# Kernel tuning notes

Hardware: AMD Instinct MI355X
Metric: run time of the kernel (lower is better)

The kernel has to match this reference:

```python
import jax, jax.numpy as jnp
import numpy as np

B, T, C = 1, 4096, 1024
NH, NKV, HD = 16, 4, 64
N_REP = NH // NKV
WIN = 1024
EPS = 1e-5
ROPE_THETA = 10000.0


def setup_inputs() -> dict:
    key = jax.random.key(0)
    ks = jax.random.split(key, 6)
    s = 1.0 / np.sqrt(C)
    x = jax.random.normal(ks[0], (B, T, C), jnp.float32)
    wq = jax.random.normal(ks[1], (NH * HD, C), jnp.float32) * s
    wk = jax.random.normal(ks[2], (NKV * HD, C), jnp.float32) * s
    wv = jax.random.normal(ks[3], (NKV * HD, C), jnp.float32) * s
    wo = jax.random.normal(ks[4], (C, NH * HD), jnp.float32) * (1.0 / np.sqrt(NH * HD))
    q_norm_w = jnp.ones((HD,), jnp.float32)
    k_norm_w = jnp.ones((HD,), jnp.float32)
    # RoPE tables: (T, HD//2)
    inv_freq = 1.0 / (ROPE_THETA ** (np.arange(0, HD, 2, dtype=np.float32) / HD))
    ang = np.outer(np.arange(T, dtype=np.float32), inv_freq)
    freqs_cos = jnp.asarray(np.cos(ang), jnp.float32)
    freqs_sin = jnp.asarray(np.sin(ang), jnp.float32)
    return {"x": x, "wq": wq, "wk": wk, "wv": wv, "wo": wo,
            "q_norm_w": q_norm_w, "k_norm_w": k_norm_w,
            "freqs_cos": freqs_cos, "freqs_sin": freqs_sin}


def _rmsnorm(v, w):
    # RMSNorm over last dim (per-head)
    return v * jax.lax.rsqrt(jnp.mean(v * v, axis=-1, keepdims=True) + EPS) * w


def _rope(v, cos, sin):
    # v: (B, T, H, HD); interleaved complex rotation, matching torch polar freqs_cis
    vr, vi = v[..., 0::2], v[..., 1::2]
    c = cos[None, :, None, :]
    s = sin[None, :, None, :]
    out_r = vr * c - vi * s
    out_i = vr * s + vi * c
    return jnp.stack([out_r, out_i], axis=-1).reshape(v.shape)


def reference(x, wq, wk, wv, wo, q_norm_w, k_norm_w, freqs_cos, freqs_sin):
    xq = jnp.einsum('btc,dc->btd', x, wq).reshape(B, T, NH, HD)
    xk = jnp.einsum('btc,dc->btd', x, wk).reshape(B, T, NKV, HD)
    xv = jnp.einsum('btc,dc->btd', x, wv).reshape(B, T, NKV, HD)
    # per-head QK RMSNorm
    xq = _rmsnorm(xq, q_norm_w)
    xk = _rmsnorm(xk, k_norm_w)
    # RoPE
    xq = _rope(xq, freqs_cos, freqs_sin)
    xk = _rope(xk, freqs_cos, freqs_sin)
    # GQA: expand kv heads
    xk = jnp.repeat(xk, N_REP, axis=2)  # (B, T, NH, HD)
    xv = jnp.repeat(xv, N_REP, axis=2)
    scale = 1.0 / np.sqrt(HD)
    scores = jnp.einsum('bthd,bshd->bhts', xq, xk) * scale
    i = jnp.arange(T)[:, None]
    j = jnp.arange(T)[None, :]
    mask = (i >= j) & (i - j < WIN)  # causal + sliding window
    scores = jnp.where(mask[None, None], scores, -jnp.inf)
    attn = jax.nn.softmax(scores, axis=-1)
    y = jnp.einsum('bhts,bshd->bthd', attn, xv).reshape(B, T, NH * HD)
    return jnp.einsum('btd,cd->btc', y, wo)
```

## Files before the change

### kernel.cpp

```cpp
#include <hip/hip_runtime.h>
#include <hip/hip_bf16.h>


#define WIN_SZ 1024

typedef __attribute__((ext_vector_type(8))) short short8;
typedef __attribute__((ext_vector_type(8))) unsigned short ushort8;
typedef __attribute__((ext_vector_type(4))) float f32x4;
typedef __attribute__((ext_vector_type(16))) float f32x16;

#define GLOAD_LDS16(g, s)                                              \
  __builtin_amdgcn_global_load_lds(                                    \
      (const __attribute__((address_space(1))) unsigned int*)(g),      \
      (__attribute__((address_space(3))) unsigned int*)(s), 16, 0, 0)

__device__ __forceinline__ unsigned short f2bf(float f) {
  union { float f; unsigned u; } v; v.f = f;
  unsigned r = v.u + 0x7fffu + ((v.u >> 16) & 1u);
  return (unsigned short)(r >> 16);
}

__device__ __forceinline__ unsigned pk2bf(float lo, float hi) {
  __hip_bfloat162 h = __float22bfloat162_rn(make_float2(lo, hi));
  union { __hip_bfloat162 h; unsigned u; } c; c.h = h; return c.u;
}

__device__ __forceinline__ short8 frag4(unsigned w0, unsigned w1, unsigned w2, unsigned w3) {
  union { unsigned u[4]; short8 s; } x;
  x.u[0] = w0; x.u[1] = w1; x.u[2] = w2; x.u[3] = w3; return x.s;
}

__global__ __launch_bounds__(256) void k_f2b_all(const float* __restrict__ x,
                                                 const float* __restrict__ wq,
                                                 const float* __restrict__ wk,
                                                 const float* __restrict__ wv,
                                                 const float* __restrict__ wo,
                                                 unsigned short* __restrict__ xb,
                                                 unsigned short* __restrict__ wqkvb,
                                                 unsigned short* __restrict__ wob) {
  int q = blockIdx.x * 256 + threadIdx.x;
  const float* src;
  unsigned short* dst;
  int off;
  if (q < 1048576) { src = x; dst = xb; off = q; }
  else if (q < 1310720) { src = wq; dst = wqkvb; off = q - 1048576; }
  else if (q < 1376256) { src = wk; dst = wqkvb + 1024 * 1024; off = q - 1310720; }
  else if (q < 1441792) { src = wv; dst = wqkvb + 1280 * 1024; off = q - 1376256; }
  else { src = wo; dst = wob; off = q - 1441792; }
  float4 v = ((const float4*)src)[off];
  ushort4 o;
  o.x = f2bf(v.x); o.y = f2bf(v.y); o.z = f2bf(v.z); o.w = f2bf(v.w);
  ((ushort4*)dst)[off] = o;
}

__global__ __launch_bounds__(256) void k_gemm_qkv(const unsigned short* __restrict__ A,
                                                  const unsigned short* __restrict__ B,
                                                  const float* __restrict__ qw,
                                                  const float* __restrict__ kw,
                                                  const float* __restrict__ fc,
                                                  const float* __restrict__ fs,
                                                  unsigned short* __restrict__ Qb,
                                                  unsigned short* __restrict__ Kb,
                                                  unsigned short* __restrict__ Vtg) {
  const int K = 1024;
  __shared__ unsigned short As[2][128 * 64];
  __shared__ unsigned short Bs[2][64 * 64];
  const int id = blockIdx.x;
  const int chunk = gridDim.x >> 3;
  const int swz = (id & 7) * chunk + (id >> 3);
  const int n_idx = swz % 24, m_idx = swz / 24;
  const int m0 = m_idx * 128, n0 = n_idx * 64;

  const int tid = threadIdx.x;
  const int w = tid >> 6, l = tid & 63;
  const int wr = w >> 1, wc = w & 1;
  const int r = l & 15, g = l >> 4;
  const int lr = l >> 3, lc = l & 7;
  const int srowb = w * 32, browb = w * 16;

  f32x4 acc[4][2];
#pragma unroll
  for (int i = 0; i < 4; i++)
#pragma unroll
    for (int j = 0; j < 2; j++) acc[i][j] = {0.f, 0.f, 0.f, 0.f};

  const unsigned short* Ag = A + (size_t)(m0 + srowb + lr) * K + lc * 8;
  const unsigned short* Bg = B + (size_t)(n0 + browb + lr) * K + lc * 8;

  auto stage = [&](int buf, int k0) {
#pragma unroll
    for (int it = 0; it < 4; it++)
      GLOAD_LDS16(Ag + (size_t)(it * 8) * K + k0, &As[buf][(srowb + it * 8) * 64]);
#pragma unroll
    for (int it = 0; it < 2; it++)
      GLOAD_LDS16(Bg + (size_t)(it * 8) * K + k0, &Bs[buf][(browb + it * 8) * 64]);
  };

  stage(0, 0);
  __syncthreads();
  int cur = 0;
  const int NT = K >> 6;
  for (int t = 0; t < NT; ++t) {
    if (t + 1 < NT) stage(cur ^ 1, (t + 1) << 6);
    const char* Ab = (const char*)As[cur];
    const char* Bb = (const char*)Bs[cur];
#pragma unroll
    for (int kk = 0; kk < 2; kk++) {
      short8 af[4], bfr[2];
#pragma unroll
      for (int mi = 0; mi < 4; mi++)
        af[mi] = *(const short8*)(Ab + (wr * 64 + mi * 16 + r) * 128 + kk * 64 + g * 16);
#pragma unroll
      for (int nj = 0; nj < 2; nj++)
        bfr[nj] = *(const short8*)(Bb + (wc * 32 + nj * 16 + r) * 128 + kk * 64 + g * 16);
#pragma unroll
      for (int mi = 0; mi < 4; mi++)
#pragma unroll
        for (int nj = 0; nj < 2; nj++)
          acc[mi][nj] = __builtin_amdgcn_mfma_f32_16x16x32_bf16(af[mi], bfr[nj], acc[mi][nj], 0, 0, 0);
    }
    __syncthreads();
    cur ^= 1;
  }

  const int u = n0 >> 6;
  if (u < 20) {
    float* ssb = (float*)As;
    f32x4 sv[4];
#pragma unroll
    for (int mi = 0; mi < 4; mi++) {
      f32x4 s;
#pragma unroll
      for (int e = 0; e < 4; e++)
        s[e] = acc[mi][0][e] * acc[mi][0][e] + acc[mi][1][e] * acc[mi][1][e];
#pragma unroll
      for (int off = 1; off < 16; off <<= 1)
#pragma unroll
        for (int e = 0; e < 4; e++) s[e] += __shfl_xor(s[e], off);
      sv[mi] = s;
    }
    if (r == 0) {
#pragma unroll
      for (int mi = 0; mi < 4; mi++)
#pragma unroll
        for (int e = 0; e < 4; e++)
          ssb[(wr * 64 + mi * 16 + g * 4 + e) * 2 + wc] = sv[mi][e];
    }
    __syncthreads();
    const float escale = (u < 16) ? 0.1803368801111204f : 1.0f;
    const float* wgt = (u < 16) ? qw : kw;
#pragma unroll
    for (int mi = 0; mi < 4; mi++) {
      const int rl0 = wr * 64 + mi * 16 + g * 4;
      const int row0 = m0 + rl0;
#pragma unroll
      for (int e = 0; e < 4; e++) {
        const int row = row0 + e;
        float ss = ssb[(rl0 + e) * 2] + ssb[(rl0 + e) * 2 + 1];
        float rms = rsqrtf(ss * (1.0f / 64.0f) + 1e-5f);
#pragma unroll
        for (int nj = 0; nj < 2; nj++) {
          const int cl = wc * 32 + nj * 16 + r;
          float vn = acc[mi][nj][e] * rms * wgt[cl];
          float c = fc[row * 32 + (cl >> 1)];
          float s = fs[row * 32 + (cl >> 1)];
          float pvn = __shfl_xor(vn, 1);
          float outv = (cl & 1) ? (pvn * s + vn * c) : (vn * c - pvn * s);
          unsigned short ob = f2bf(outv * escale);
          if (u < 16) Qb[(size_t)row * 1024 + n0 + cl] = ob;
          else Kb[(size_t)row * 256 + (n0 - 1024) + cl] = ob;
        }
      }
    }
  } else {
#pragma unroll
    for (int mi = 0; mi < 4; mi++) {
      const int row0 = m0 + wr * 64 + mi * 16 + g * 4;
#pragma unroll
      for (int nj = 0; nj < 2; nj++) {
        const int d = (n0 - 1280) + wc * 32 + nj * 16 + r;
        ushort4 ov;
        ov.x = f2bf(acc[mi][nj][0]);
        ov.y = f2bf(acc[mi][nj][1]);
        ov.z = f2bf(acc[mi][nj][2]);
        ov.w = f2bf(acc[mi][nj][3]);
        *(ushort4*)(Vtg + (size_t)d * 4096 + row0) = ov;
      }
    }
  }
}

__global__ __launch_bounds__(256) void k_gemm_out(const unsigned short* __restrict__ A,
                                                  const unsigned short* __restrict__ B,
                                                  float* __restrict__ C) {
  const int K = 1024, N = 1024;
  __shared__ unsigned short As[2][128 * 64];
  __shared__ unsigned short Bs[2][64 * 64];
  const int id = blockIdx.x;
  const int chunk = gridDim.x >> 3;
  const int swz = (id & 7) * chunk + (id >> 3);
  const int n_idx = swz % 16, m_idx = swz / 16;
  const int m0 = m_idx * 128, n0 = n_idx * 64;

  const int tid = threadIdx.x;
  const int w = tid >> 6, l = tid & 63;
  const int wr = w >> 1, wc = w & 1;
  const int r = l & 15, g = l >> 4;
  const int lr = l >> 3, lc = l & 7;
  const int srowb = w * 32, browb = w * 16;

  f32x4 acc[4][2];
#pragma unroll
  for (int i = 0; i < 4; i++)
#pragma unroll
    for (int j = 0; j < 2; j++) acc[i][j] = {0.f, 0.f, 0.f, 0.f};

  const unsigned short* Ag = A + (size_t)(m0 + srowb + lr) * K + lc * 8;
  const unsigned short* Bg = B + (size_t)(n0 + browb + lr) * K + lc * 8;

  auto stage = [&](int buf, int k0) {
#pragma unroll
    for (int it = 0; it < 4; it++)
      GLOAD_LDS16(Ag + (size_t)(it * 8) * K + k0, &As[buf][(srowb + it * 8) * 64]);
#pragma unroll
    for (int it = 0; it < 2; it++)
      GLOAD_LDS16(Bg + (size_t)(it * 8) * K + k0, &Bs[buf][(browb + it * 8) * 64]);
  };

  stage(0, 0);
  __syncthreads();
  int cur = 0;
  const int NT = K >> 6;
  for (int t = 0; t < NT; ++t) {
    if (t + 1 < NT) stage(cur ^ 1, (t + 1) << 6);
    const char* Ab = (const char*)As[cur];
    const char* Bb = (const char*)Bs[cur];
#pragma unroll
    for (int kk = 0; kk < 2; kk++) {
      short8 af[4], bfr[2];
#pragma unroll
      for (int mi = 0; mi < 4; mi++)
        af[mi] = *(const short8*)(Ab + (wr * 64 + mi * 16 + r) * 128 + kk * 64 + g * 16);
#pragma unroll
      for (int nj = 0; nj < 2; nj++)
        bfr[nj] = *(const short8*)(Bb + (wc * 32 + nj * 16 + r) * 128 + kk * 64 + g * 16);
#pragma unroll
      for (int mi = 0; mi < 4; mi++)
#pragma unroll
        for (int nj = 0; nj < 2; nj++)
          acc[mi][nj] = __builtin_amdgcn_mfma_f32_16x16x32_bf16(af[mi], bfr[nj], acc[mi][nj], 0, 0, 0);
    }
    __syncthreads();
    cur ^= 1;
  }

#pragma unroll
  for (int mi = 0; mi < 4; mi++)
#pragma unroll
    for (int nj = 0; nj < 2; nj++) {
      int row = m0 + wr * 64 + mi * 16 + g * 4;
      int col = n0 + wc * 32 + nj * 16 + r;
#pragma unroll
      for (int e = 0; e < 4; e++)
        C[(size_t)(row + e) * N + col] = acc[mi][nj][e];
    }
}

__global__ __launch_bounds__(512, 4) void k_attn9(const unsigned short* __restrict__ Qb,
                                                  const unsigned short* __restrict__ Kb,
                                                  const unsigned short* __restrict__ Vtg,
                                                  unsigned short* __restrict__ Yb) {
  __shared__ char smem[57344];
  char* stage = smem;
  float* Obuf = (float*)smem;
  float* ml = (float*)(smem + 32768);

  const int id = blockIdx.x;
  const int cupair = id & 255, sel = id >> 8;
  int qi = cupair >> 1;
  if (sel) qi = 127 - qi;
  const int hk = (cupair & 1) * 2 + sel;
  const int q0 = qi * 32;

  const int tid = threadIdx.x, w = tid >> 6, l = tid & 63;
  const int hh = w & 3, half = w >> 2;
  const int h = hk * 4 + hh;
  const int l31 = l & 31, hi = l >> 5, l15 = l & 15;
  const int qrow = q0 + l31;

  int jlo = q0 - (WIN_SZ - 1);
  if (jlo < 0) jlo = 0;
  jlo &= ~63;
  const int jlast = ((q0 + 31) >> 6) << 6;
  const int nt = ((jlast - jlo) >> 6) + 1;
  const int nh0 = (nt + 1) >> 1;

  const int sb = tid >> 7;
  const int su = tid & 127;
  const int srow = su >> 1;
  const int sg = (su & 1) * 4;
  const int sbase = sb * 8192 + (srow & 31) * 256;
  const int srx = (srow & 15) << 4;
  const int srh = (srow >> 5) * 128;
  const bool isV = sb & 1;
  const unsigned short* gK = Kb + (size_t)srow * 256 + hk * 64 + sg * 8;
  const unsigned short* gV = Vtg + (size_t)(hk * 64 + srow) * 4096 + sg * 8;

  short8 qf[4];
#pragma unroll
  for (int ks = 0; ks < 4; ks++)
    qf[ks] = *(const short8*)(Qb + (size_t)qrow * 1024 + h * 64 + ks * 16 + hi * 8);

  const short8 ones = frag4(0x3F803F80u, 0x3F803F80u, 0x3F803F80u, 0x3F803F80u);

  f32x16 accO0, accO1;
#pragma unroll
  for (int i = 0; i < 16; i++) { accO0[i] = 0.f; accO1[i] = 0.f; }
  float m = -1e30f, lsum = 0.f;

  ushort8 pre[4];
  auto prefetch = [&](int s) {
    int jt0 = jlo + (s << 6);
    int t1 = nh0 + s;
    int jt1 = (t1 < nt) ? (jlo + (t1 << 6)) : jlo;
    int jt = (sb >= 2) ? jt1 : jt0;
    if (!isV) {
      const unsigned short* g = gK + (size_t)jt * 256;
#pragma unroll
      for (int e = 0; e < 4; e++) pre[e] = *(const ushort8*)(g + e * 8);
    } else {
      const unsigned short* g = gV + jt;
#pragma unroll
      for (int e = 0; e < 4; e++) pre[e] = *(const ushort8*)(g + e * 8);
    }
  };
  prefetch(0);

  const int kbase = half * 16384;
  const int vbase = kbase + 8192;

  for (int s = 0; s < nh0; ++s) {
    __syncthreads();
#pragma unroll
    for (int e = 0; e < 4; e++) {
      int dst = sbase + ((srh + (sg + e) * 16) ^ srx);
      *(ushort8*)(stage + dst) = pre[e];
    }
    __syncthreads();
    if (s + 1 < nh0) prefetch(s + 1);

    const int myt = half ? (nh0 + s) : s;
    if (myt < nt) {
      const int jt = jlo + (myt << 6);

      f32x16 st0, st1;
#pragma unroll
      for (int i = 0; i < 16; i++) { st0[i] = 0.f; st1[i] = 0.f; }
      __builtin_amdgcn_s_setprio(1);
#pragma unroll
      for (int ks = 0; ks < 4; ks++) {
        int colb = ks * 32 + hi * 16;
        short8 kf0 = *(const short8*)(stage + kbase + l31 * 256 + (colb ^ (l15 << 4)));
        st0 = __builtin_amdgcn_mfma_f32_32x32x16_bf16(kf0, qf[ks], st0, 0, 0, 0);
        short8 kf1 = *(const short8*)(stage + kbase + l31 * 256 + ((128 + colb) ^ (l15 << 4)));
        st1 = __builtin_amdgcn_mfma_f32_32x32x16_bf16(kf1, qf[ks], st1, 0, 0, 0);
      }
      __builtin_amdgcn_s_setprio(0);

      if (jt + 63 > q0 || (q0 + 31) - jt >= WIN_SZ) {
        const int jb = jt + hi * 4;
#pragma unroll
        for (int rg = 0; rg < 16; rg++) {
          int j0 = jb + (rg & 3) + 8 * (rg >> 2);
          if (!((j0 <= qrow) && (qrow - j0 < WIN_SZ))) st0[rg] = -3.0e38f;
          int j1 = j0 + 32;
          if (!((j1 <= qrow) && (qrow - j1 < WIN_SZ))) st1[rg] = -3.0e38f;
        }
      }

      float mx = st0[0];
#pragma unroll
      for (int rg = 1; rg < 16; rg++) mx = fmaxf(mx, st0[rg]);
#pragma unroll
      for (int rg = 0; rg < 16; rg++) mx = fmaxf(mx, st1[rg]);
      mx = fmaxf(mx, __shfl_xor(mx, 32));
      if (!__all(mx <= m + 8.0f)) {
        float mnew = fmaxf(m, mx);
        float alpha = exp2f(m - mnew);
#pragma unroll
        for (int rg = 0; rg < 16; rg++) { accO0[rg] *= alpha; accO1[rg] *= alpha; }
        lsum *= alpha;
        m = mnew;
      }
#pragma unroll
      for (int rg = 0; rg < 16; rg++) st0[rg] = exp2f(st0[rg] - m);
#pragma unroll
      for (int rg = 0; rg < 16; rg++) st1[rg] = exp2f(st1[rg] - m);

      unsigned pd0[2][4], pd1[2][4];
#pragma unroll
      for (int b = 0; b < 4; b++) {
        pd0[0][b] = pk2bf(st0[4 * b], st0[4 * b + 1]);
        pd1[0][b] = pk2bf(st0[4 * b + 2], st0[4 * b + 3]);
        pd0[1][b] = pk2bf(st1[4 * b], st1[4 * b + 1]);
        pd1[1][b] = pk2bf(st1[4 * b + 2], st1[4 * b + 3]);
      }

      f32x16 accL;
#pragma unroll
      for (int i = 0; i < 16; i++) accL[i] = 0.f;

      __builtin_amdgcn_s_setprio(1);
#pragma unroll
      for (int jj = 0; jj < 2; jj++) {
#pragma unroll
        for (int ks2 = 0; ks2 < 2; ks2++) {
          unsigned a0 = pd0[jj][2 * ks2], a1 = pd0[jj][2 * ks2 + 1];
          unsigned b0 = pd1[jj][2 * ks2], b1 = pd1[jj][2 * ks2 + 1];
          unsigned a0x = __shfl_xor(a0, 32), a1x = __shfl_xor(a1, 32);
          unsigned b0x = __shfl_xor(b0, 32), b1x = __shfl_xor(b1, 32);
          unsigned w0 = hi ? a1x : a0;
          unsigned w1 = hi ? b1x : b0;
          unsigned w2 = hi ? a1 : a0x;
          unsigned w3 = hi ? b1 : b0x;
          short8 pf = frag4(w0, w1, w2, w3);
          int colb2 = jj * 64 + ks2 * 32 + hi * 16;
          short8 vf0 = *(const short8*)(stage + vbase + l31 * 256 + (colb2 ^ (l15 << 4)));
          accO0 = __builtin_amdgcn_mfma_f32_32x32x16_bf16(vf0, pf, accO0, 0, 0, 0);
          short8 vf1 = *(const short8*)(stage + vbase + l31 * 256 + ((128 + colb2) ^ (l15 << 4)));
          accO1 = __builtin_amdgcn_mfma_f32_32x32x16_bf16(vf1, pf, accO1, 0, 0, 0);
          accL = __builtin_amdgcn_mfma_f32_32x32x16_bf16(ones, pf, accL, 0, 0, 0);
        }
      }
      __builtin_amdgcn_s_setprio(0);
      lsum += accL[0];
    }
  }

  __syncthreads();
  if (half == 1) {
#pragma unroll
    for (int dd = 0; dd < 2; dd++) {
      const f32x16& a = dd ? accO1 : accO0;
#pragma unroll
      for (int rg = 0; rg < 16; rg++) {
        int d = dd * 32 + 8 * (rg >> 2) + 4 * hi + (rg & 3);
        Obuf[(hh * 64 + d) * 32 + l31] = a[rg];
      }
    }
    if (!hi) { ml[(hh * 2 + 0) * 32 + l31] = m; ml[(hh * 2 + 1) * 32 + l31] = lsum; }
  }
  __syncthreads();
  if (half == 0) {
    float m1 = ml[(hh * 2 + 0) * 32 + l31];
    float l1 = ml[(hh * 2 + 1) * 32 + l31];
    float ms = fmaxf(m, m1);
    float a0 = exp2f(m - ms), a1 = exp2f(m1 - ms);
    float inv = 1.0f / (lsum * a0 + l1 * a1);
    a0 *= inv; a1 *= inv;
#pragma unroll
    for (int dd = 0; dd < 2; dd++) {
      const f32x16& a = dd ? accO1 : accO0;
#pragma unroll
      for (int b = 0; b < 4; b++) {
        float o[4];
#pragma unroll
        for (int e = 0; e < 4; e++) {
          int d = dd * 32 + 8 * b + 4 * hi + e;
          o[e] = a[4 * b + e] * a0 + Obuf[(hh * 64 + d) * 32 + l31] * a1;
        }
        union { unsigned uu[2]; ushort4 v; } ov;
        ov.uu[0] = pk2bf(o[0], o[1]);
        ov.uu[1] = pk2bf(o[2], o[3]);
        *(ushort4*)(Yb + (size_t)qrow * 1024 + h * 64 + dd * 32 + b * 8 + hi * 4) = ov.v;
      }
    }
  }
}

extern "C" void kernel_launch(void* const* d_in, const int* in_sizes, int n_in,
                              void* d_out, int out_size, void* d_ws, size_t ws_size,
                              hipStream_t stream) {
  const float* x = (const float*)d_in[0];
  const float* wq = (const float*)d_in[1];
  const float* wk = (const float*)d_in[2];
  const float* wv = (const float*)d_in[3];
  const float* wo = (const float*)d_in[4];
  const float* qw = (const float*)d_in[5];
  const float* kw = (const float*)d_in[6];
  const float* fc = (const float*)d_in[7];
  const float* fs = (const float*)d_in[8];
  float* out = (float*)d_out;

  char* p = (char*)d_ws;
  auto alloc = [&](size_t b) {
    char* q = p;
    p += (b + 255) & ~(size_t)255;
    return q;
  };
  unsigned short* xb = (unsigned short*)alloc((size_t)4096 * 1024 * 2);
  unsigned short* wqkvb = (unsigned short*)alloc((size_t)1536 * 1024 * 2);
  unsigned short* wob = (unsigned short*)alloc((size_t)1024 * 1024 * 2);
  unsigned short* Qb = (unsigned short*)alloc((size_t)4096 * 1024 * 2);
  unsigned short* Kb = (unsigned short*)alloc((size_t)4096 * 256 * 2);
  unsigned short* Vtg = (unsigned short*)alloc((size_t)256 * 4096 * 2);
  unsigned short* Yb = (unsigned short*)alloc((size_t)4096 * 1024 * 2);

  k_f2b_all<<<6656, 256, 0, stream>>>(x, wq, wk, wv, wo, xb, wqkvb, wob);
  k_gemm_qkv<<<768, 256, 0, stream>>>(xb, wqkvb, qw, kw, fc, fs, Qb, Kb, Vtg);
  k_attn9<<<512, 512, 0, stream>>>(Qb, Kb, Vtg, Yb);
  k_gemm_out<<<512, 256, 0, stream>>>(Yb, wob, out);
}
```

Baseline: 108.2 us.

## Split attention KV range four ways per block with tree merge of partials

The attention kernel now launches 1024-thread blocks in which four wave groups each handle a quarter of the KV tiles, up from two halves. Each group stages its own K/V tile in shared memory, and the partial softmax states are combined afterwards through a two-level tree merge in LDS. This roughly halves the serial tile loop length per block and adds more waves to hide latency. In exchange it uses more LDS and registers per block, adds extra barrier rounds for the merge, and leaves more idle groups when the tile count is small, as in early causal rows.

```diff
diff --git a/kernel.cpp b/kernel.cpp
--- a/kernel.cpp
+++ b/kernel.cpp
@@ -266,14 +266,15 @@
     }
 }
 
-__global__ __launch_bounds__(512, 4) void k_attn9(const unsigned short* __restrict__ Qb,
-                                                  const unsigned short* __restrict__ Kb,
-                                                  const unsigned short* __restrict__ Vtg,
-                                                  unsigned short* __restrict__ Yb) {
-  __shared__ char smem[57344];
+__global__ __launch_bounds__(1024, 8) void k_attn11(const unsigned short* __restrict__ Qb,
+                                                    const unsigned short* __restrict__ Kb,
+                                                    const unsigned short* __restrict__ Vtg,
+                                                    unsigned short* __restrict__ Yb) {
+  __shared__ char smem[65536 + 3072];
   char* stage = smem;
-  float* Obuf = (float*)smem;
-  float* ml = (float*)(smem + 32768);
+  float* Obuf0 = (float*)smem;
+  float* Obuf1 = (float*)(smem + 32768);
+  float* mlr = (float*)(smem + 65536);
 
   const int id = blockIdx.x;
   const int cupair = id & 255, sel = id >> 8;
@@ -283,7 +284,7 @@
   const int q0 = qi * 32;
 
   const int tid = threadIdx.x, w = tid >> 6, l = tid & 63;
-  const int hh = w & 3, half = w >> 2;
+  const int hh = w & 3, qr = w >> 2;
   const int h = hk * 4 + hh;
   const int l31 = l & 31, hi = l >> 5, l15 = l & 15;
   const int qrow = q0 + l31;
@@ -293,16 +294,17 @@
   jlo &= ~63;
   const int jlast = ((q0 + 31) >> 6) << 6;
   const int nt = ((jlast - jlo) >> 6) + 1;
-  const int nh0 = (nt + 1) >> 1;
+  const int nq = (nt + 3) >> 2;
 
   const int sb = tid >> 7;
+  const int qr_s = sb >> 1;
+  const bool isV = sb & 1;
   const int su = tid & 127;
   const int srow = su >> 1;
   const int sg = (su & 1) * 4;
   const int sbase = sb * 8192 + (srow & 31) * 256;
   const int srx = (srow & 15) << 4;
   const int srh = (srow >> 5) * 128;
-  const bool isV = sb & 1;
   const unsigned short* gK = Kb + (size_t)srow * 256 + hk * 64 + sg * 8;
   const unsigned short* gV = Vtg + (size_t)(hk * 64 + srow) * 4096 + sg * 8;
 
@@ -318,12 +320,11 @@
   for (int i = 0; i < 16; i++) { accO0[i] = 0.f; accO1[i] = 0.f; }
   float m = -1e30f, lsum = 0.f;
 
+  const int tend_s = min((qr_s + 1) * nq, nt);
   ushort8 pre[4];
   auto prefetch = [&](int s) {
-    int jt0 = jlo + (s << 6);
-    int t1 = nh0 + s;
-    int jt1 = (t1 < nt) ? (jlo + (t1 << 6)) : jlo;
-    int jt = (sb >= 2) ? jt1 : jt0;
+    int t = qr_s * nq + s;
+    int jt = (t < tend_s) ? (jlo + (t << 6)) : jlo;
     if (!isV) {
       const unsigned short* g = gK + (size_t)jt * 256;
 #pragma unroll
@@ -336,10 +337,12 @@
   };
   prefetch(0);
 
-  const int kbase = half * 16384;
+  const int kbase = qr * 2 * 8192;
   const int vbase = kbase + 8192;
-
-  for (int s = 0; s < nh0; ++s) {
+  const int tq0 = qr * nq;
+  const int tqe = min(tq0 + nq, nt);
+
+  for (int s = 0; s < nq; ++s) {
     __syncthreads();
 #pragma unroll
     for (int e = 0; e < 4; e++) {
@@ -347,10 +350,10 @@
       *(ushort8*)(stage + dst) = pre[e];
     }
     __syncthreads();
-    if (s + 1 < nh0) prefetch(s + 1);
-
-    const int myt = half ? (nh0 + s) : s;
-    if (myt < nt) {
+    if (s + 1 < nq) prefetch(s + 1);
+
+    const int myt = tq0 + s;
+    if (myt < tqe) {
       const int jt = jlo + (myt << 6);
 
       f32x16 st0, st1;
@@ -437,41 +440,59 @@
     }
   }
 
-  __syncthreads();
-  if (half == 1) {
+  auto publish = [&](float* Ob, int src) {
 #pragma unroll
     for (int dd = 0; dd < 2; dd++) {
       const f32x16& a = dd ? accO1 : accO0;
 #pragma unroll
       for (int rg = 0; rg < 16; rg++) {
         int d = dd * 32 + 8 * (rg >> 2) + 4 * hi + (rg & 3);
-        Obuf[(hh * 64 + d) * 32 + l31] = a[rg];
-      }
-    }
-    if (!hi) { ml[(hh * 2 + 0) * 32 + l31] = m; ml[(hh * 2 + 1) * 32 + l31] = lsum; }
-  }
-  __syncthreads();
-  if (half == 0) {
-    float m1 = ml[(hh * 2 + 0) * 32 + l31];
-    float l1 = ml[(hh * 2 + 1) * 32 + l31];
+        Ob[(hh * 64 + d) * 32 + l31] = a[rg];
+      }
+    }
+    if (!hi) {
+      mlr[(src * 2 + 0) * 128 + hh * 32 + l31] = m;
+      mlr[(src * 2 + 1) * 128 + hh * 32 + l31] = lsum;
+    }
+  };
+  auto merge_from = [&](const float* Ob, int src) {
+    float m1 = mlr[(src * 2 + 0) * 128 + hh * 32 + l31];
+    float l1 = mlr[(src * 2 + 1) * 128 + hh * 32 + l31];
     float ms = fmaxf(m, m1);
     float a0 = exp2f(m - ms), a1 = exp2f(m1 - ms);
-    float inv = 1.0f / (lsum * a0 + l1 * a1);
-    a0 *= inv; a1 *= inv;
+#pragma unroll
+    for (int dd = 0; dd < 2; dd++) {
+      f32x16& a = dd ? accO1 : accO0;
+#pragma unroll
+      for (int rg = 0; rg < 16; rg++) {
+        int d = dd * 32 + 8 * (rg >> 2) + 4 * hi + (rg & 3);
+        a[rg] = a[rg] * a0 + Ob[(hh * 64 + d) * 32 + l31] * a1;
+      }
+    }
+    lsum = lsum * a0 + l1 * a1;
+    m = ms;
+  };
+
+  __syncthreads();
+  if (qr == 1) publish(Obuf0, 0);
+  if (qr == 3) publish(Obuf1, 1);
+  __syncthreads();
+  if (qr == 0) merge_from(Obuf0, 0);
+  if (qr == 2) merge_from(Obuf1, 1);
+  __syncthreads();
+  if (qr == 2) publish(Obuf0, 2);
+  __syncthreads();
+  if (qr == 0) {
+    merge_from(Obuf0, 2);
+    float inv = 1.0f / lsum;
 #pragma unroll
     for (int dd = 0; dd < 2; dd++) {
       const f32x16& a = dd ? accO1 : accO0;
 #pragma unroll
       for (int b = 0; b < 4; b++) {
-        float o[4];
-#pragma unroll
-        for (int e = 0; e < 4; e++) {
-          int d = dd * 32 + 8 * b + 4 * hi + e;
-          o[e] = a[4 * b + e] * a0 + Obuf[(hh * 64 + d) * 32 + l31] * a1;
-        }
         union { unsigned uu[2]; ushort4 v; } ov;
-        ov.uu[0] = pk2bf(o[0], o[1]);
-        ov.uu[1] = pk2bf(o[2], o[3]);
+        ov.uu[0] = pk2bf(a[4 * b] * inv, a[4 * b + 1] * inv);
+        ov.uu[1] = pk2bf(a[4 * b + 2] * inv, a[4 * b + 3] * inv);
         *(ushort4*)(Yb + (size_t)qrow * 1024 + h * 64 + dd * 32 + b * 8 + hi * 4) = ov.v;
       }
     }
@@ -508,6 +529,6 @@
 
   k_f2b_all<<<6656, 256, 0, stream>>>(x, wq, wk, wv, wo, xb, wqkvb, wob);
   k_gemm_qkv<<<768, 256, 0, stream>>>(xb, wqkvb, qw, kw, fc, fs, Qb, Kb, Vtg);
-  k_attn9<<<512, 512, 0, stream>>>(Qb, Kb, Vtg, Yb);
+  k_attn11<<<512, 1024, 0, stream>>>(Qb, Kb, Vtg, Yb);
   k_gemm_out<<<512, 256, 0, stream>>>(Yb, wob, out);
 }
```

New measurement: 325.6 us. 201% more time.
